# Optimization experiments

Measured on AMD Instinct MI355X. Metric: run time of the kernel, lower is better.

Reference implementation:

```python
import jax, jax.numpy as jnp
import numpy as np

T, B, I, H = 4096, 64, 128, 1024


def setup_inputs() -> dict:
    key = jax.random.key(0)
    k1, k2, k3, k4, k5 = jax.random.split(key, 5)
    # scale recurrent/input weights so tanh doesn't saturate (ESN-style init)
    x = jax.random.normal(k1, (T, B, I), dtype=jnp.float32)
    weight_ih = jax.random.normal(k2, (H, I), dtype=jnp.float32) / np.sqrt(I)
    weight_hh = jax.random.normal(k3, (H, H), dtype=jnp.float32) * (0.9 / np.sqrt(H))
    bias_ih = jax.random.normal(k4, (H,), dtype=jnp.float32) * 0.1
    bias_hh = jax.random.normal(k5, (H,), dtype=jnp.float32) * 0.1
    return {"x": x, "weight_ih": weight_ih, "weight_hh": weight_hh,
            "bias_ih": bias_ih, "bias_hh": bias_hh}


def reference(x, weight_ih, weight_hh, bias_ih, bias_hh):
    # ESN recurrence: h_t = tanh(x_t @ Wih^T + b_ih + h_{t-1} @ Whh^T + b_hh)
    # x: [T, B, I]; returns final hidden state hx: [B, H]
    def step(h, xt):
        pre = xt @ weight_ih.T + bias_ih + h @ weight_hh.T + bias_hh
        h_new = jnp.tanh(pre)
        return h_new, None

    h0 = jnp.zeros((x.shape[1], weight_hh.shape[0]), dtype=x.dtype)
    h_final, _ = jax.lax.scan(step, h0, x)
    return h_final
```

## Files before the change

### kernel.cpp

```cpp
#include <hip/hip_runtime.h>


#define TT 4096
#define BB 64
#define II 128
#define HH 1024

typedef _Float16 f16x8 __attribute__((ext_vector_type(8)));
typedef float f32x4 __attribute__((ext_vector_type(4)));
typedef unsigned int u32x4 __attribute__((ext_vector_type(4)));

static __device__ __forceinline__ unsigned short f2h_bits(float f) {
    _Float16 h = (_Float16)f;
    return __builtin_bit_cast(unsigned short, h);
}

static __device__ __forceinline__ u32x4 gload16_sc1(const unsigned int* p) {
    u32x4 r;
    asm volatile("global_load_dwordx4 %0, %1, off sc1"
                 : "=v"(r) : "v"(p) : "memory");
    return r;
}

__device__ __forceinline__ int swz(int L) {
    return (L & 0x78) | (((L & 7) + (L >> 3)) & 7);
}

__global__ __launch_bounds__(256, 1) void esn_kernel(
    const float* __restrict__ x, const float* __restrict__ wih,
    const float* __restrict__ whh, const float* __restrict__ bih,
    const float* __restrict__ bhh, float* __restrict__ out,
    unsigned int* __restrict__ hbu0, unsigned int* __restrict__ hbu1,
    unsigned int* __restrict__ flags)
{
    __shared__ __align__(16) unsigned short h_lds[16 * 1032];
    __shared__ __align__(16) unsigned short x_lds[16 * 136];
    __shared__ __align__(16) unsigned int   c_lds[16 * 36];

    const int tid  = threadIdx.x;
    const int lane = tid & 63;
    const int wv   = tid >> 6;
    const int col  = lane & 15;
    const int quad = lane >> 4;

    const int blk    = blockIdx.x;
    const int m      = blk >> 4;
    const int m_base = m * 16;
    const int jj     = blk & 15;
    const int n_idx  = jj * 4 + wv;
    const int n_base = n_idx * 16;

    f16x8 wh[32], wi[4];
#pragma unroll
    for (int kt = 0; kt < 32; ++kt) {
        const float* p = whh + (size_t)(n_base + col) * HH + kt * 32 + quad * 8;
        f16x8 w;
#pragma unroll
        for (int j = 0; j < 8; ++j) w[j] = (_Float16)p[j];
        wh[kt] = w;
    }
#pragma unroll
    for (int kt = 0; kt < 4; ++kt) {
        const float* p = wih + (size_t)(n_base + col) * II + kt * 32 + quad * 8;
        f16x8 w;
#pragma unroll
        for (int j = 0; j < 8; ++j) w[j] = (_Float16)p[j];
        wi[kt] = w;
    }
    const float bias_sum = bih[n_base + col] + bhh[n_base + col];

    const int sr = tid >> 4;
    const int sc = tid & 15;
    const int csrc = tid >> 4;
    const int crow = tid & 15;
    const unsigned int* fl = flags + m * 16;

    f32x4 xa, xb;
    {
        const float* gp = x + (size_t)(m_base + sr) * II + sc * 8;
        xa = *(const f32x4*)gp;
        xb = *(const f32x4*)(gp + 4);
    }

    for (int t = 0; t < TT; ++t) {
        const unsigned int* rbu = (t & 1) ? hbu1 : hbu0;
        unsigned int*       wbu = (t & 1) ? hbu0 : hbu1;

        {
            f16x8 v;
#pragma unroll
            for (int j = 0; j < 4; ++j) v[j] = (_Float16)xa[j];
#pragma unroll
            for (int j = 0; j < 4; ++j) v[4 + j] = (_Float16)xb[j];
            *(f16x8*)(x_lds + sr * 136 + sc * 8) = v;
        }

        if (wv == 0) {
            const bool skip = (lane >= 16);
            const unsigned int* fp = fl + lane;
            for (;;) {
                unsigned int v = 0;
                if (!skip)
                    asm volatile("global_load_dword %0, %1, off sc1\n\t"
                                 "s_waitcnt vmcnt(0)"
                                 : "=v"(v) : "v"(fp) : "memory");
                if (__ballot(skip || v >= (unsigned int)t) == ~0ull) break;
            }
        }
        __syncthreads();

        {
            const unsigned int* gp = rbu + (size_t)(m * 16 + csrc) * 512 + crow * 32;
            u32x4 a0 = gload16_sc1(gp);
            u32x4 a1 = gload16_sc1(gp + 4);
            u32x4 a2 = gload16_sc1(gp + 8);
            u32x4 a3 = gload16_sc1(gp + 12);
            u32x4 a4 = gload16_sc1(gp + 16);
            u32x4 a5 = gload16_sc1(gp + 20);
            u32x4 a6 = gload16_sc1(gp + 24);
            u32x4 a7 = gload16_sc1(gp + 28);
            asm volatile("s_waitcnt vmcnt(0)"
                         : "+v"(a0), "+v"(a1), "+v"(a2), "+v"(a3),
                           "+v"(a4), "+v"(a5), "+v"(a6), "+v"(a7)
                         :: "memory");
            unsigned short* lp = h_lds + crow * 1032;
            *(u32x4*)(lp + swz(csrc * 8 + 0) * 8) = a0;
            *(u32x4*)(lp + swz(csrc * 8 + 1) * 8) = a1;
            *(u32x4*)(lp + swz(csrc * 8 + 2) * 8) = a2;
            *(u32x4*)(lp + swz(csrc * 8 + 3) * 8) = a3;
            *(u32x4*)(lp + swz(csrc * 8 + 4) * 8) = a4;
            *(u32x4*)(lp + swz(csrc * 8 + 5) * 8) = a5;
            *(u32x4*)(lp + swz(csrc * 8 + 6) * 8) = a6;
            *(u32x4*)(lp + swz(csrc * 8 + 7) * 8) = a7;
        }
        __syncthreads();

        if (t + 1 < TT) {
            const float* gp = x + (size_t)(t + 1) * (BB * II)
                              + (size_t)(m_base + sr) * II + sc * 8;
            xa = *(const f32x4*)gp;
            xb = *(const f32x4*)(gp + 4);
        }

        f32x4 acc0 = {0.f, 0.f, 0.f, 0.f};
        f32x4 acc1 = {0.f, 0.f, 0.f, 0.f};
        const unsigned short* arow = h_lds + col * 1032;
#pragma unroll
        for (int kt = 0; kt < 32; ++kt) {
            f16x8 a = *(const f16x8*)(arow + swz(kt * 4 + quad) * 8);
            ((kt & 1) ? acc1 : acc0) =
                __builtin_amdgcn_mfma_f32_16x16x32_f16(
                    a, wh[kt], ((kt & 1) ? acc1 : acc0), 0, 0, 0);
        }
        const unsigned short* xrow = x_lds + col * 136;
#pragma unroll
        for (int kt = 0; kt < 4; ++kt) {
            f16x8 a = *(const f16x8*)(xrow + kt * 32 + quad * 8);
            ((kt & 1) ? acc1 : acc0) =
                __builtin_amdgcn_mfma_f32_16x16x32_f16(
                    a, wi[kt], ((kt & 1) ? acc1 : acc0), 0, 0, 0);
        }

        float th[4];
#pragma unroll
        for (int i = 0; i < 4; ++i) {
            float pre = acc0[i] + acc1[i] + bias_sum;
            float pc  = fminf(fmaxf(pre, -9.f), 9.f);
            float e   = __expf(2.f * pc);
            th[i] = (e - 1.f) / (e + 1.f);
        }
        {
            unsigned int p01 = (unsigned int)f2h_bits(th[0]) |
                               ((unsigned int)f2h_bits(th[1]) << 16);
            unsigned int p23 = (unsigned int)f2h_bits(th[2]) |
                               ((unsigned int)f2h_bits(th[3]) << 16);
            unsigned int q01 = (unsigned int)__shfl_xor((int)p01, 1, 64);
            unsigned int q23 = (unsigned int)__shfl_xor((int)p23, 1, 64);
            if (!(lane & 1)) {
                unsigned int w0 = (p01 & 0xFFFFu) | (q01 << 16);
                unsigned int w1 = (p01 >> 16) | (q01 & 0xFFFF0000u);
                unsigned int w2 = (p23 & 0xFFFFu) | (q23 << 16);
                unsigned int w3 = (p23 >> 16) | (q23 & 0xFFFF0000u);
                const int c = wv * 8 + (col >> 1);
                unsigned int* cl = c_lds + (quad * 4) * 36 + c;
                cl[0]      = w0;
                cl[36]     = w1;
                cl[2 * 36] = w2;
                cl[3 * 36] = w3;
            }
        }
        if (t == TT - 1) {
#pragma unroll
            for (int i = 0; i < 4; ++i)
                out[(size_t)(m_base + quad * 4 + i) * HH + n_base + col] = th[i];
        }
        __syncthreads();

        if (t < TT - 1) {
            const int r  = tid >> 4;
            const int c0 = (tid & 15) * 2;
            unsigned int* dst = wbu + (size_t)(m * 16 + jj) * 512 + r * 32 + c0;
            atomicExch(dst,     c_lds[r * 36 + c0]);
            atomicExch(dst + 1, c_lds[r * 36 + c0 + 1]);
            asm volatile("s_waitcnt vmcnt(0)" ::: "memory");
            __syncthreads();
            if (tid == 0)
                atomicExch(&flags[m * 16 + jj], (unsigned int)(t + 1));
        }
    }
}

extern "C" void kernel_launch(void* const* d_in, const int* in_sizes, int n_in,
                              void* d_out, int out_size, void* d_ws, size_t ws_size,
                              hipStream_t stream) {
    const float* x   = (const float*)d_in[0];
    const float* wih = (const float*)d_in[1];
    const float* whh = (const float*)d_in[2];
    const float* bih = (const float*)d_in[3];
    const float* bhh = (const float*)d_in[4];
    float* out = (float*)d_out;

    unsigned int* hbu0  = (unsigned int*)d_ws;
    unsigned int* hbu1  = hbu0 + 32768;
    unsigned int* flags = (unsigned int*)((char*)d_ws + 262144);

    hipMemsetAsync(d_ws, 0, 262144 + 256, stream);

    esn_kernel<<<dim3(64), dim3(256), 0, stream>>>(x, wih, whh, bih, bhh,
                                                   out, hbu0, hbu1, flags);
}
```

Measured before the change: 16.16 ms.

## Pad sync flags to 128B lines, relayout hidden LDS tile, use four accumulators

Each block's progress flag now sits on its own 128-byte stride, so the per-step polling and flag writes no longer contend on a shared cache line. The hidden-state LDS tile changes from a swizzled row-major layout to a k-chunk-major layout where each MFMA A-fragment read is contiguous, which removes the swizzle arithmetic. The recurrent MFMA chain is split across four accumulators instead of two to shorten dependency stalls. The risks are extra workspace for the flags and possible LDS bank conflicts on the new strided writes.

```diff
diff --git a/kernel.cpp b/kernel.cpp
--- a/kernel.cpp
+++ b/kernel.cpp
@@ -20,10 +20,6 @@
     asm volatile("global_load_dwordx4 %0, %1, off sc1"
                  : "=v"(r) : "v"(p) : "memory");
     return r;
-}
-
-__device__ __forceinline__ int swz(int L) {
-    return (L & 0x78) | (((L & 7) + (L >> 3)) & 7);
 }
 
 __global__ __launch_bounds__(256, 1) void esn_kernel(
@@ -33,7 +29,7 @@
     unsigned int* __restrict__ hbu0, unsigned int* __restrict__ hbu1,
     unsigned int* __restrict__ flags)
 {
-    __shared__ __align__(16) unsigned short h_lds[16 * 1032];
+    __shared__ __align__(16) unsigned short h_lds[128 * 16 * 8];
     __shared__ __align__(16) unsigned short x_lds[16 * 136];
     __shared__ __align__(16) unsigned int   c_lds[16 * 36];
 
@@ -69,11 +65,11 @@
     }
     const float bias_sum = bih[n_base + col] + bhh[n_base + col];
 
-    const int sr = tid >> 4;
-    const int sc = tid & 15;
+    const int sr   = tid >> 4;
+    const int sc   = tid & 15;
     const int csrc = tid >> 4;
     const int crow = tid & 15;
-    const unsigned int* fl = flags + m * 16;
+    const unsigned int* fl = flags + m * 512;
 
     f32x4 xa, xb;
     {
@@ -97,7 +93,7 @@
 
         if (wv == 0) {
             const bool skip = (lane >= 16);
-            const unsigned int* fp = fl + lane;
+            const unsigned int* fp = fl + lane * 32;
             for (;;) {
                 unsigned int v = 0;
                 if (!skip)
@@ -123,15 +119,15 @@
                          : "+v"(a0), "+v"(a1), "+v"(a2), "+v"(a3),
                            "+v"(a4), "+v"(a5), "+v"(a6), "+v"(a7)
                          :: "memory");
-            unsigned short* lp = h_lds + crow * 1032;
-            *(u32x4*)(lp + swz(csrc * 8 + 0) * 8) = a0;
-            *(u32x4*)(lp + swz(csrc * 8 + 1) * 8) = a1;
-            *(u32x4*)(lp + swz(csrc * 8 + 2) * 8) = a2;
-            *(u32x4*)(lp + swz(csrc * 8 + 3) * 8) = a3;
-            *(u32x4*)(lp + swz(csrc * 8 + 4) * 8) = a4;
-            *(u32x4*)(lp + swz(csrc * 8 + 5) * 8) = a5;
-            *(u32x4*)(lp + swz(csrc * 8 + 6) * 8) = a6;
-            *(u32x4*)(lp + swz(csrc * 8 + 7) * 8) = a7;
+            unsigned short* lp = h_lds + crow * 8;
+            *(u32x4*)(lp + (csrc * 8 + 0) * 128) = a0;
+            *(u32x4*)(lp + (csrc * 8 + 1) * 128) = a1;
+            *(u32x4*)(lp + (csrc * 8 + 2) * 128) = a2;
+            *(u32x4*)(lp + (csrc * 8 + 3) * 128) = a3;
+            *(u32x4*)(lp + (csrc * 8 + 4) * 128) = a4;
+            *(u32x4*)(lp + (csrc * 8 + 5) * 128) = a5;
+            *(u32x4*)(lp + (csrc * 8 + 6) * 128) = a6;
+            *(u32x4*)(lp + (csrc * 8 + 7) * 128) = a7;
         }
         __syncthreads();
 
@@ -142,29 +138,28 @@
             xb = *(const f32x4*)(gp + 4);
         }
 
-        f32x4 acc0 = {0.f, 0.f, 0.f, 0.f};
-        f32x4 acc1 = {0.f, 0.f, 0.f, 0.f};
-        const unsigned short* arow = h_lds + col * 1032;
+        f32x4 acc[4];
+#pragma unroll
+        for (int i = 0; i < 4; ++i) acc[i] = (f32x4){0.f, 0.f, 0.f, 0.f};
 #pragma unroll
         for (int kt = 0; kt < 32; ++kt) {
-            f16x8 a = *(const f16x8*)(arow + swz(kt * 4 + quad) * 8);
-            ((kt & 1) ? acc1 : acc0) =
-                __builtin_amdgcn_mfma_f32_16x16x32_f16(
-                    a, wh[kt], ((kt & 1) ? acc1 : acc0), 0, 0, 0);
+            f16x8 a = *(const f16x8*)(h_lds + (4 * kt + quad) * 128 + col * 8);
+            acc[kt & 3] = __builtin_amdgcn_mfma_f32_16x16x32_f16(
+                a, wh[kt], acc[kt & 3], 0, 0, 0);
         }
         const unsigned short* xrow = x_lds + col * 136;
 #pragma unroll
         for (int kt = 0; kt < 4; ++kt) {
             f16x8 a = *(const f16x8*)(xrow + kt * 32 + quad * 8);
-            ((kt & 1) ? acc1 : acc0) =
-                __builtin_amdgcn_mfma_f32_16x16x32_f16(
-                    a, wi[kt], ((kt & 1) ? acc1 : acc0), 0, 0, 0);
+            acc[kt & 3] = __builtin_amdgcn_mfma_f32_16x16x32_f16(
+                a, wi[kt], acc[kt & 3], 0, 0, 0);
         }
 
         float th[4];
 #pragma unroll
         for (int i = 0; i < 4; ++i) {
-            float pre = acc0[i] + acc1[i] + bias_sum;
+            float pre = (acc[0][i] + acc[1][i]) + (acc[2][i] + acc[3][i])
+                        + bias_sum;
             float pc  = fminf(fmaxf(pre, -9.f), 9.f);
             float e   = __expf(2.f * pc);
             th[i] = (e - 1.f) / (e + 1.f);
@@ -205,7 +200,8 @@
             asm volatile("s_waitcnt vmcnt(0)" ::: "memory");
             __syncthreads();
             if (tid == 0)
-                atomicExch(&flags[m * 16 + jj], (unsigned int)(t + 1));
+                atomicExch((unsigned int*)(flags + (m * 16 + jj) * 32),
+                           (unsigned int)(t + 1));
         }
     }
 }
@@ -224,7 +220,7 @@
     unsigned int* hbu1  = hbu0 + 32768;
     unsigned int* flags = (unsigned int*)((char*)d_ws + 262144);
 
-    hipMemsetAsync(d_ws, 0, 262144 + 256, stream);
+    hipMemsetAsync(d_ws, 0, 262144 + 8192, stream);
 
     esn_kernel<<<dim3(64), dim3(256), 0, stream>>>(x, wih, whh, bih, bhh,
                                                    out, hbu0, hbu1, flags);
```

New measurement: 15.45 ms. 4.3% less time.
